# Performance work log

Hardware: AMD Instinct MI355X
Metric: run time of the kernel (lower is better)

## Reference

```python
import jax, jax.numpy as jnp
import numpy as np

B, N, D = 8, 2048, 128
NEG = -9.0e15


def setup_inputs() -> dict:
    key = jax.random.key(0)
    ks = jax.random.split(key, 7)
    x = jax.random.normal(ks[0], (B, N, D), dtype=jnp.float32)
    # sparse-ish binary adjacency with self loops, stored dense as float
    adj = (jax.random.uniform(ks[1], (B, N, N)) < 0.1).astype(jnp.float32)
    adj = jnp.maximum(adj, jnp.eye(N, dtype=jnp.float32)[None])
    s = 1.0 / np.sqrt(D)
    W_w = jax.random.uniform(ks[2], (D, D), minval=-s, maxval=s, dtype=jnp.float32)
    W_b = jax.random.uniform(ks[3], (D,), minval=-s, maxval=s, dtype=jnp.float32)
    A = jnp.zeros((D, D), dtype=jnp.float32) + 0.01 * jax.random.normal(ks[4], (D, D), dtype=jnp.float32)
    s2 = 1.0 / np.sqrt(2 * D)
    gate_w = jax.random.uniform(ks[5], (1, 2 * D), minval=-s2, maxval=s2, dtype=jnp.float32)
    gate_b = jax.random.uniform(ks[6], (1,), minval=-s2, maxval=s2, dtype=jnp.float32)
    return {"x": x, "adj": adj, "W_w": W_w, "W_b": W_b, "A": A,
            "gate_w": gate_w, "gate_b": gate_b}


def reference(x, adj, W_w, W_b, A, gate_w, gate_b):
    # h = W(x): [B,N,D]
    h = jnp.einsum('bnf,df->bnd', x, W_w) + W_b
    # e[b,j,k] = (h A)[b,j,:] . h[b,k,:], then symmetrize
    hA = jnp.einsum('bnd,de->bne', h, A)
    e = jnp.einsum('bjl,bkl->bjk', hA, h)
    e = e + jnp.swapaxes(e, 1, 2)
    att = jnp.where(adj > 0, e, jnp.full_like(e, NEG))
    # NOTE: torch code softmaxes over dim=1 (the j axis)
    att = jax.nn.softmax(att, axis=1)
    att = att * adj
    h_prime = jax.nn.relu(jnp.einsum('bij,bjk->bik', att, h))
    gate_in = jnp.concatenate([x, h_prime], axis=-1)  # [B,N,2D]
    coeff = jax.nn.sigmoid(jnp.einsum('bnc,oc->bno', gate_in, gate_w) + gate_b)  # [B,N,1]
    return coeff * x + (1.0 - coeff) * h_prime
```

## Files before the change

kernel.cpp:

```cpp
#include <hip/hip_runtime.h>


#define B_ 8
#define N_ 2048
#define D_ 128

typedef __attribute__((ext_vector_type(8))) short short8;
typedef __attribute__((ext_vector_type(4))) float f32x4;

#define GLL(gp, lp) __builtin_amdgcn_global_load_lds( \
    (__attribute__((address_space(1))) const unsigned int*)(gp), \
    (__attribute__((address_space(3))) unsigned int*)(lp), 16, 0, 0)

static __device__ __forceinline__ unsigned short f2bf(float f) {
  union { float f; unsigned int u; } v; v.f = f;
  unsigned int r = v.u + 0x7fffu + ((v.u >> 16) & 1u);
  return (unsigned short)(r >> 16);
}
static __device__ __forceinline__ float bf2f(unsigned short u) {
  union { unsigned int u; float f; } v; v.u = ((unsigned int)u) << 16;
  return v.f;
}

#define CAT_OFF ((size_t)0)
#define VT_OFF  ((size_t)8388608)
#define PUN_OFF ((size_t)12582912)
#define S_OFF   ((size_t)79691776)
#define WT_OFF  ((size_t)79757312)

__global__ void k_wt(const float* __restrict__ W, float* __restrict__ Wt) {
  int t = threadIdx.x;
  for (int i = t; i < 128 * 128; i += 256) {
    int d = i >> 7, f = i & 127;
    Wt[f * 128 + d] = W[i];
  }
}

__global__ __launch_bounds__(256) void k1(const float* __restrict__ x,
                                          const float* __restrict__ Wt,
                                          const float* __restrict__ Wb,
                                          const float* __restrict__ A,
                                          unsigned short* __restrict__ cat) {
  __shared__ float xs[8][128];
  __shared__ float hs[8][128];
  const int t = threadIdx.x;
  const size_t rowbase = (size_t)blockIdx.x * 8;
  {
    int row = t >> 5, part = t & 31;
    *(f32x4*)&xs[row][part * 4] = *(const f32x4*)(x + (rowbase + row) * D_ + part * 4);
  }
  __syncthreads();
  const int d = t & 127, r2 = t >> 7;
  float a0 = 0, a1 = 0, a2 = 0, a3 = 0;
  for (int f = 0; f < 128; f++) {
    float wv = Wt[f * 128 + d];
    a0 += xs[r2 * 4 + 0][f] * wv;
    a1 += xs[r2 * 4 + 1][f] * wv;
    a2 += xs[r2 * 4 + 2][f] * wv;
    a3 += xs[r2 * 4 + 3][f] * wv;
  }
  float wb = Wb[d];
  a0 += wb; a1 += wb; a2 += wb; a3 += wb;
  hs[r2 * 4 + 0][d] = a0; hs[r2 * 4 + 1][d] = a1;
  hs[r2 * 4 + 2][d] = a2; hs[r2 * 4 + 3][d] = a3;
  cat[(rowbase + r2 * 4 + 0) * 256 + 128 + d] = f2bf(a0);
  cat[(rowbase + r2 * 4 + 1) * 256 + 128 + d] = f2bf(a1);
  cat[(rowbase + r2 * 4 + 2) * 256 + 128 + d] = f2bf(a2);
  cat[(rowbase + r2 * 4 + 3) * 256 + 128 + d] = f2bf(a3);
  __syncthreads();
  float b0 = 0, b1 = 0, b2 = 0, b3 = 0;
  for (int f = 0; f < 128; f++) {
    float av = A[f * 128 + d];
    b0 += hs[r2 * 4 + 0][f] * av;
    b1 += hs[r2 * 4 + 1][f] * av;
    b2 += hs[r2 * 4 + 2][f] * av;
    b3 += hs[r2 * 4 + 3][f] * av;
  }
  cat[(rowbase + r2 * 4 + 0) * 256 + d] = f2bf(b0);
  cat[(rowbase + r2 * 4 + 1) * 256 + d] = f2bf(b1);
  cat[(rowbase + r2 * 4 + 2) * 256 + d] = f2bf(b2);
  cat[(rowbase + r2 * 4 + 3) * 256 + d] = f2bf(b3);
}

__global__ __launch_bounds__(256, 3) void k2(const unsigned short* __restrict__ cat,
                                             const float* __restrict__ adj,
                                             unsigned short* __restrict__ pun,
                                             float* __restrict__ s_out) {
  __shared__ unsigned short cj[64 * 256];
  const int t = threadIdx.x, w = t >> 6, lane = t & 63;
  const int q = lane >> 4, l15 = lane & 15;
  const int b = blockIdx.z;
  const int kbase = blockIdx.x * 128;
  const int j0b = blockIdx.y * 128;
  const size_t bN = (size_t)b * N_;
  const unsigned short* catp = cat + (bN << 8);
  const int kc = kbase + w * 32;
  short8 brg[2][8];
#pragma unroll
  for (int p = 0; p < 2; p++) {
    int krow = kc + 2 * l15 + p;
#pragma unroll
    for (int m = 0; m < 8; m++)
      brg[p][m] = *(const short8*)(catp + (((size_t)krow) << 8) +
                                   ((((m * 4 + q) + 16) & 31) * 8));
  }
  float acc0 = 0.f, acc1 = 0.f;
  for (int jt = 0; jt < 2; jt++) {
    const int j0 = j0b + jt * 64;
#pragma unroll
    for (int it = 0; it < 8; it++) {
      int sI = it * 256 + t;
      int row = sI >> 5, c = sI & 31;
      GLL(catp + (((size_t)(j0 + row)) << 8) + (c ^ (row & 7)) * 8,
          (char*)cj + sI * 16);
    }
    __syncthreads();
#pragma unroll
    for (int jsub = 0; jsub < 4; jsub++) {
      float2 av[4];
#pragma unroll
      for (int r = 0; r < 4; r++) {
        int jrow = j0 + jsub * 16 + q * 4 + r;
        av[r] = *(const float2*)(adj + (((size_t)(bN + jrow)) << 11) + kc + 2 * l15);
      }
      const int row = jsub * 16 + l15;
      short8 afr[8];
#pragma unroll
      for (int m = 0; m < 8; m++)
        afr[m] = *(short8*)(cj + row * 256 + (((m * 4 + q) ^ (l15 & 7)) * 8));
      f32x4 e0 = {0.f, 0.f, 0.f, 0.f}, e1 = {0.f, 0.f, 0.f, 0.f};
#pragma unroll
      for (int m = 0; m < 8; m++) {
        e0 = __builtin_amdgcn_mfma_f32_16x16x32_bf16(afr[m], brg[0][m], e0, 0, 0, 0);
        e1 = __builtin_amdgcn_mfma_f32_16x16x32_bf16(afr[m], brg[1][m], e1, 0, 0, 0);
      }
#pragma unroll
      for (int r = 0; r < 4; r++) {
        int jrow = j0 + jsub * 16 + q * 4 + r;
        float x0 = av[r].x > 0.f ? __expf(fminf(e0[r], 60.f)) : 0.f;
        float x1 = av[r].y > 0.f ? __expf(fminf(e1[r], 60.f)) : 0.f;
        acc0 += x0; acc1 += x1;
        unsigned int pk = (unsigned int)f2bf(x0) | ((unsigned int)f2bf(x1) << 16);
        *(unsigned int*)(pun + (((size_t)(bN + jrow)) << 11) + kc + 2 * l15) = pk;
      }
    }
    __syncthreads();
  }
  acc0 += __shfl_xor(acc0, 16, 64); acc0 += __shfl_xor(acc0, 32, 64);
  acc1 += __shfl_xor(acc1, 16, 64); acc1 += __shfl_xor(acc1, 32, 64);
  if (lane < 16) {
    atomicAdd(&s_out[bN + kc + 2 * lane], acc0);
    atomicAdd(&s_out[bN + kc + 2 * lane + 1], acc1);
  }
}

__global__ __launch_bounds__(256) void k1v(const unsigned short* __restrict__ cat,
                                           const float* __restrict__ s,
                                           unsigned short* __restrict__ vt) {
  __shared__ unsigned short tile[64][136];
  __shared__ float rsv[64];
  const int t = threadIdx.x;
  const int b = blockIdx.y;
  const int nbase = blockIdx.x * 64;
  if (t < 64) rsv[t] = 1.f / s[(size_t)b * N_ + nbase + t];
#pragma unroll
  for (int k = 0; k < 4; k++) {
    int sI = t + 256 * k;
    int row = sI >> 4, part = sI & 15;
    *(short8*)&tile[row][part * 8] =
        *(const short8*)(cat + (((size_t)(b * N_ + nbase + row)) << 8) + 128 + part * 8);
  }
  __syncthreads();
#pragma unroll
  for (int k = 0; k < 4; k++) {
    int sI = t + 256 * k;
    int dd = sI >> 3, part = sI & 7;
    unsigned short tmp[8];
#pragma unroll
    for (int j = 0; j < 8; j++) {
      int jj = part * 8 + j;
      tmp[j] = f2bf(bf2f(tile[jj][dd]) * rsv[jj]);
    }
    *(short8*)(vt + (((size_t)(b * 128 + dd)) << 11) + nbase + part * 8) = *(short8*)tmp;
  }
}

__global__ __launch_bounds__(256) void k3(const unsigned short* __restrict__ pun,
                                          const unsigned short* __restrict__ vt,
                                          const float* __restrict__ x,
                                          const float* __restrict__ gw,
                                          const float* __restrict__ gb,
                                          float* __restrict__ out) {
  __shared__ char smem[40960];
  const int t = threadIdx.x, w = t >> 6, lane = t & 63;
  const int q = lane >> 4, l15 = lane & 15;
  const int b = blockIdx.y, i0 = blockIdx.x * 32;
  const size_t bN = (size_t)b * N_;
  unsigned short* pa = (unsigned short*)smem;
  unsigned short* vb = (unsigned short*)(smem + 8192);

  f32x4 acc[2][2];
#pragma unroll
  for (int ih = 0; ih < 2; ih++)
#pragma unroll
    for (int dh = 0; dh < 2; dh++) acc[ih][dh] = (f32x4){0.f, 0.f, 0.f, 0.f};

  for (int jt = 0; jt < N_ / 128; jt++) {
    const int j0 = jt * 128;
#pragma unroll
    for (int it = 0; it < 10; it++) {
      int sI = it * 256 + t;
      const unsigned short* g;
      if (sI < 512) {
        int row = sI >> 4, c = sI & 15;
        g = pun + (((size_t)(bN + i0 + row)) << 11) + j0 + ((c ^ (row & 7)) * 8);
      } else {
        int s2 = sI - 512;
        int dd = s2 >> 4, c = s2 & 15;
        g = vt + (((size_t)(b * 128 + dd)) << 11) + j0 + ((c ^ (dd & 7)) * 8);
      }
      GLL(g, smem + sI * 16);
    }
    __syncthreads();
#pragma unroll
    for (int ks = 0; ks < 4; ks++) {
      short8 af[2], bf[2];
#pragma unroll
      for (int ih = 0; ih < 2; ih++) {
        int m = ih * 16 + l15;
        af[ih] = *(short8*)(pa + m * 128 + (((ks * 4 + q) ^ (m & 7)) * 8));
      }
#pragma unroll
      for (int dh = 0; dh < 2; dh++) {
        int d = w * 32 + dh * 16 + l15;
        bf[dh] = *(short8*)(vb + d * 128 + (((ks * 4 + q) ^ (d & 7)) * 8));
      }
      acc[0][0] = __builtin_amdgcn_mfma_f32_16x16x32_bf16(af[0], bf[0], acc[0][0], 0, 0, 0);
      acc[0][1] = __builtin_amdgcn_mfma_f32_16x16x32_bf16(af[0], bf[1], acc[0][1], 0, 0, 0);
      acc[1][0] = __builtin_amdgcn_mfma_f32_16x16x32_bf16(af[1], bf[0], acc[1][0], 0, 0, 0);
      acc[1][1] = __builtin_amdgcn_mfma_f32_16x16x32_bf16(af[1], bf[1], acc[1][1], 0, 0, 0);
    }
    __syncthreads();
  }
  float* hs = (float*)smem;
  float* co = (float*)(smem + 16896);
#pragma unroll
  for (int ih = 0; ih < 2; ih++)
#pragma unroll
    for (int dh = 0; dh < 2; dh++)
#pragma unroll
      for (int r = 0; r < 4; r++) {
        int row = ih * 16 + q * 4 + r;
        int d = w * 32 + dh * 16 + l15;
        hs[row * 132 + d] = fmaxf(acc[ih][dh][r], 0.f);
      }
  __syncthreads();
  {
    int grow = t >> 3, sub = t & 7;
    const float* xr = x + (((size_t)(bN + i0 + grow)) << 7);
    float z = 0.f;
#pragma unroll
    for (int k = 0; k < 16; k++) {
      int dd = sub + 8 * k;
      z += gw[dd] * xr[dd] + gw[128 + dd] * hs[grow * 132 + dd];
    }
    z += __shfl_xor(z, 1, 64);
    z += __shfl_xor(z, 2, 64);
    z += __shfl_xor(z, 4, 64);
    if (sub == 0) co[grow] = 1.f / (1.f + __expf(-(z + gb[0])));
  }
  __syncthreads();
#pragma unroll
  for (int kk = 0; kk < 4; kk++) {
    int id = kk * 256 + t;
    int row = id >> 5, c4 = id & 31;
    size_t g = (((size_t)(bN + i0 + row)) << 7) + c4 * 4;
    f32x4 xv = *(const f32x4*)(x + g);
    f32x4 hv = *(const f32x4*)(hs + row * 132 + c4 * 4);
    float cf = co[row];
    f32x4 o;
#pragma unroll
    for (int e = 0; e < 4; e++) o[e] = cf * xv[e] + (1.f - cf) * hv[e];
    *(f32x4*)(out + g) = o;
  }
}

extern "C" void kernel_launch(void* const* d_in, const int* in_sizes, int n_in,
                              void* d_out, int out_size, void* d_ws, size_t ws_size,
                              hipStream_t stream) {
  const float* x   = (const float*)d_in[0];
  const float* adj = (const float*)d_in[1];
  const float* Ww  = (const float*)d_in[2];
  const float* Wb  = (const float*)d_in[3];
  const float* A   = (const float*)d_in[4];
  const float* gw  = (const float*)d_in[5];
  const float* gb  = (const float*)d_in[6];
  float* out = (float*)d_out;
  char* ws = (char*)d_ws;

  unsigned short* cat = (unsigned short*)(ws + CAT_OFF);
  unsigned short* vt  = (unsigned short*)(ws + VT_OFF);
  unsigned short* pun = (unsigned short*)(ws + PUN_OFF);
  float* s  = (float*)(ws + S_OFF);
  float* Wt = (float*)(ws + WT_OFF);

  hipMemsetAsync(s, 0, (size_t)B_ * N_ * sizeof(float), stream);
  k_wt<<<1, 256, 0, stream>>>(Ww, Wt);
  k1<<<(B_ * N_) / 8, 256, 0, stream>>>(x, Wt, Wb, A, cat);
  k2<<<dim3(N_ / 128, 16, B_), 256, 0, stream>>>(cat, adj, pun, s);
  k1v<<<dim3(N_ / 64, B_), 256, 0, stream>>>(cat, s, vt);
  k3<<<dim3(N_ / 32, B_), 256, 0, stream>>>(pun, vt, x, gw, gb, out);
}
```

Baseline: 310.0 us.

## Drop LDS staging in k2, read j-rows directly and prefetch adjacency

```diff
diff --git a/kernel.cpp b/kernel.cpp
--- a/kernel.cpp
+++ b/kernel.cpp
@@ -82,69 +82,58 @@
   cat[(rowbase + r2 * 4 + 3) * 256 + d] = f2bf(b3);
 }
 
-__global__ __launch_bounds__(256, 3) void k2(const unsigned short* __restrict__ cat,
-                                             const float* __restrict__ adj,
-                                             unsigned short* __restrict__ pun,
-                                             float* __restrict__ s_out) {
-  __shared__ unsigned short cj[64 * 256];
+__global__ __launch_bounds__(256) void k2(const unsigned short* __restrict__ cat,
+                                          const float* __restrict__ adj,
+                                          unsigned short* __restrict__ pun,
+                                          float* __restrict__ s_out) {
   const int t = threadIdx.x, w = t >> 6, lane = t & 63;
   const int q = lane >> 4, l15 = lane & 15;
   const int b = blockIdx.z;
-  const int kbase = blockIdx.x * 128;
-  const int j0b = blockIdx.y * 128;
+  const int kc = (blockIdx.x * 4 + w) * 32;
+  const int j0 = blockIdx.y * 128;
   const size_t bN = (size_t)b * N_;
   const unsigned short* catp = cat + (bN << 8);
-  const int kc = kbase + w * 32;
   short8 brg[2][8];
 #pragma unroll
-  for (int p = 0; p < 2; p++) {
-    int krow = kc + 2 * l15 + p;
+  for (int p = 0; p < 2; p++)
 #pragma unroll
     for (int m = 0; m < 8; m++)
-      brg[p][m] = *(const short8*)(catp + (((size_t)krow) << 8) +
+      brg[p][m] = *(const short8*)(catp + (((size_t)(kc + 2 * l15 + p)) << 8) +
                                    ((((m * 4 + q) + 16) & 31) * 8));
-  }
   float acc0 = 0.f, acc1 = 0.f;
-  for (int jt = 0; jt < 2; jt++) {
-    const int j0 = j0b + jt * 64;
-#pragma unroll
-    for (int it = 0; it < 8; it++) {
-      int sI = it * 256 + t;
-      int row = sI >> 5, c = sI & 31;
-      GLL(catp + (((size_t)(j0 + row)) << 8) + (c ^ (row & 7)) * 8,
-          (char*)cj + sI * 16);
-    }
-    __syncthreads();
-#pragma unroll
-    for (int jsub = 0; jsub < 4; jsub++) {
-      float2 av[4];
-#pragma unroll
-      for (int r = 0; r < 4; r++) {
-        int jrow = j0 + jsub * 16 + q * 4 + r;
-        av[r] = *(const float2*)(adj + (((size_t)(bN + jrow)) << 11) + kc + 2 * l15);
-      }
-      const int row = jsub * 16 + l15;
-      short8 afr[8];
-#pragma unroll
-      for (int m = 0; m < 8; m++)
-        afr[m] = *(short8*)(cj + row * 256 + (((m * 4 + q) ^ (l15 & 7)) * 8));
-      f32x4 e0 = {0.f, 0.f, 0.f, 0.f}, e1 = {0.f, 0.f, 0.f, 0.f};
-#pragma unroll
-      for (int m = 0; m < 8; m++) {
-        e0 = __builtin_amdgcn_mfma_f32_16x16x32_bf16(afr[m], brg[0][m], e0, 0, 0, 0);
-        e1 = __builtin_amdgcn_mfma_f32_16x16x32_bf16(afr[m], brg[1][m], e1, 0, 0, 0);
-      }
-#pragma unroll
-      for (int r = 0; r < 4; r++) {
-        int jrow = j0 + jsub * 16 + q * 4 + r;
-        float x0 = av[r].x > 0.f ? __expf(fminf(e0[r], 60.f)) : 0.f;
-        float x1 = av[r].y > 0.f ? __expf(fminf(e1[r], 60.f)) : 0.f;
-        acc0 += x0; acc1 += x1;
-        unsigned int pk = (unsigned int)f2bf(x0) | ((unsigned int)f2bf(x1) << 16);
-        *(unsigned int*)(pun + (((size_t)(bN + jrow)) << 11) + kc + 2 * l15) = pk;
-      }
-    }
-    __syncthreads();
+  float2 av[4];
+#pragma unroll
+  for (int r = 0; r < 4; r++)
+    av[r] = *(const float2*)(adj + ((bN + j0 + q * 4 + r) << 11) + kc + 2 * l15);
+#pragma unroll 2
+  for (int jsub = 0; jsub < 8; jsub++) {
+    const int jr = j0 + jsub * 16;
+    short8 afr[8];
+#pragma unroll
+    for (int m = 0; m < 8; m++)
+      afr[m] = *(const short8*)(catp + (((size_t)(jr + l15)) << 8) + (m * 4 + q) * 8);
+    f32x4 e0 = {0.f, 0.f, 0.f, 0.f}, e1 = {0.f, 0.f, 0.f, 0.f};
+#pragma unroll
+    for (int m = 0; m < 8; m++) {
+      e0 = __builtin_amdgcn_mfma_f32_16x16x32_bf16(afr[m], brg[0][m], e0, 0, 0, 0);
+      e1 = __builtin_amdgcn_mfma_f32_16x16x32_bf16(afr[m], brg[1][m], e1, 0, 0, 0);
+    }
+    float2 avc[4];
+#pragma unroll
+    for (int r = 0; r < 4; r++) avc[r] = av[r];
+    if (jsub < 7) {
+#pragma unroll
+      for (int r = 0; r < 4; r++)
+        av[r] = *(const float2*)(adj + ((bN + jr + 16 + q * 4 + r) << 11) + kc + 2 * l15);
+    }
+#pragma unroll
+    for (int r = 0; r < 4; r++) {
+      float x0 = avc[r].x > 0.f ? __expf(fminf(e0[r], 60.f)) : 0.f;
+      float x1 = avc[r].y > 0.f ? __expf(fminf(e1[r], 60.f)) : 0.f;
+      acc0 += x0; acc1 += x1;
+      unsigned int pk = (unsigned int)f2bf(x0) | ((unsigned int)f2bf(x1) << 16);
+      *(unsigned int*)(pun + ((bN + jr + q * 4 + r) << 11) + kc + 2 * l15) = pk;
+    }
   }
   acc0 += __shfl_xor(acc0, 16, 64); acc0 += __shfl_xor(acc0, 32, 64);
   acc1 += __shfl_xor(acc1, 16, 64); acc1 += __shfl_xor(acc1, 32, 64);
@@ -307,7 +296,7 @@
   hipMemsetAsync(s, 0, (size_t)B_ * N_ * sizeof(float), stream);
   k_wt<<<1, 256, 0, stream>>>(Ww, Wt);
   k1<<<(B_ * N_) / 8, 256, 0, stream>>>(x, Wt, Wb, A, cat);
-  k2<<<dim3(N_ / 128, 16, B_), 256, 0, stream>>>(cat, adj, pun, s);
+  k2<<<dim3(16, 16, B_), 256, 0, stream>>>(cat, adj, pun, s);
   k1v<<<dim3(N_ / 64, B_), 256, 0, stream>>>(cat, s, vt);
   k3<<<dim3(N_ / 32, B_), 256, 0, stream>>>(pun, vt, x, gw, gb, out);
 }
```

Result: slower. 349.8 us (+12.8%).

## Pack adjacency into bitmask and move projection GEMMs onto bf16 MFMA

Applied to the files above, without the earlier changes.

```diff
diff --git a/kernel.cpp b/kernel.cpp
--- a/kernel.cpp
+++ b/kernel.cpp
@@ -22,68 +22,105 @@
   return v.f;
 }
 
-#define CAT_OFF ((size_t)0)
-#define VT_OFF  ((size_t)8388608)
-#define PUN_OFF ((size_t)12582912)
-#define S_OFF   ((size_t)79691776)
-#define WT_OFF  ((size_t)79757312)
-
-__global__ void k_wt(const float* __restrict__ W, float* __restrict__ Wt) {
+#define CAT_OFF  ((size_t)0)
+#define VT_OFF   ((size_t)8388608)
+#define PUN_OFF  ((size_t)12582912)
+#define S_OFF    ((size_t)79691776)
+#define WB_OFF   ((size_t)79757312)
+#define AT_OFF   ((size_t)79790080)
+#define BITS_OFF ((size_t)79822848)
+
+__global__ void k_cvt(const float* __restrict__ W, const float* __restrict__ A,
+                      unsigned short* __restrict__ Wb1, unsigned short* __restrict__ Abt) {
   int t = threadIdx.x;
   for (int i = t; i < 128 * 128; i += 256) {
-    int d = i >> 7, f = i & 127;
-    Wt[f * 128 + d] = W[i];
-  }
+    Wb1[i] = f2bf(W[i]);
+    Abt[(i & 127) * 128 + (i >> 7)] = f2bf(A[i]);
+  }
+}
+
+__global__ __launch_bounds__(256) void k_bits2(const float* __restrict__ adj,
+                                               unsigned int* __restrict__ bits) {
+  size_t tid = (size_t)blockIdx.x * 256 + threadIdx.x;
+  const float* p = adj + tid * 32;
+  unsigned int m = 0;
+#pragma unroll
+  for (int i = 0; i < 8; i++) {
+    f32x4 v = *(const f32x4*)(p + i * 4);
+    m |= (v[0] > 0.f ? 1u : 0u) << (i * 4 + 0);
+    m |= (v[1] > 0.f ? 1u : 0u) << (i * 4 + 1);
+    m |= (v[2] > 0.f ? 1u : 0u) << (i * 4 + 2);
+    m |= (v[3] > 0.f ? 1u : 0u) << (i * 4 + 3);
+  }
+  bits[tid] = m;
 }
 
 __global__ __launch_bounds__(256) void k1(const float* __restrict__ x,
-                                          const float* __restrict__ Wt,
-                                          const float* __restrict__ Wb,
-                                          const float* __restrict__ A,
+                                          const unsigned short* __restrict__ Wb1,
+                                          const float* __restrict__ Wbias,
+                                          const unsigned short* __restrict__ Abt,
                                           unsigned short* __restrict__ cat) {
-  __shared__ float xs[8][128];
-  __shared__ float hs[8][128];
-  const int t = threadIdx.x;
-  const size_t rowbase = (size_t)blockIdx.x * 8;
-  {
-    int row = t >> 5, part = t & 31;
-    *(f32x4*)&xs[row][part * 4] = *(const f32x4*)(x + (rowbase + row) * D_ + part * 4);
-  }
-  __syncthreads();
-  const int d = t & 127, r2 = t >> 7;
-  float a0 = 0, a1 = 0, a2 = 0, a3 = 0;
-  for (int f = 0; f < 128; f++) {
-    float wv = Wt[f * 128 + d];
-    a0 += xs[r2 * 4 + 0][f] * wv;
-    a1 += xs[r2 * 4 + 1][f] * wv;
-    a2 += xs[r2 * 4 + 2][f] * wv;
-    a3 += xs[r2 * 4 + 3][f] * wv;
-  }
-  float wb = Wb[d];
-  a0 += wb; a1 += wb; a2 += wb; a3 += wb;
-  hs[r2 * 4 + 0][d] = a0; hs[r2 * 4 + 1][d] = a1;
-  hs[r2 * 4 + 2][d] = a2; hs[r2 * 4 + 3][d] = a3;
-  cat[(rowbase + r2 * 4 + 0) * 256 + 128 + d] = f2bf(a0);
-  cat[(rowbase + r2 * 4 + 1) * 256 + 128 + d] = f2bf(a1);
-  cat[(rowbase + r2 * 4 + 2) * 256 + 128 + d] = f2bf(a2);
-  cat[(rowbase + r2 * 4 + 3) * 256 + 128 + d] = f2bf(a3);
-  __syncthreads();
-  float b0 = 0, b1 = 0, b2 = 0, b3 = 0;
-  for (int f = 0; f < 128; f++) {
-    float av = A[f * 128 + d];
-    b0 += hs[r2 * 4 + 0][f] * av;
-    b1 += hs[r2 * 4 + 1][f] * av;
-    b2 += hs[r2 * 4 + 2][f] * av;
-    b3 += hs[r2 * 4 + 3][f] * av;
-  }
-  cat[(rowbase + r2 * 4 + 0) * 256 + d] = f2bf(b0);
-  cat[(rowbase + r2 * 4 + 1) * 256 + d] = f2bf(b1);
-  cat[(rowbase + r2 * 4 + 2) * 256 + d] = f2bf(b2);
-  cat[(rowbase + r2 * 4 + 3) * 256 + d] = f2bf(b3);
+  __shared__ unsigned short hsm[4][16][136];
+  __shared__ unsigned short hasm[4][16][136];
+  const int t = threadIdx.x, w = t >> 6, lane = t & 63;
+  const int q = lane >> 4, l15 = lane & 15;
+  const size_t r0 = (size_t)blockIdx.x * 64 + w * 16;
+
+  f32x4 acc[8];
+#pragma unroll
+  for (int dg = 0; dg < 8; dg++) acc[dg] = (f32x4){0.f, 0.f, 0.f, 0.f};
+#pragma unroll
+  for (int k = 0; k < 4; k++) {
+    const float* xp = x + (r0 + l15) * 128 + k * 32 + q * 8;
+    f32x4 xa = *(const f32x4*)xp;
+    f32x4 xb = *(const f32x4*)(xp + 4);
+    short8 af;
+#pragma unroll
+    for (int e = 0; e < 4; e++) { af[e] = (short)f2bf(xa[e]); af[4 + e] = (short)f2bf(xb[e]); }
+#pragma unroll
+    for (int dg = 0; dg < 8; dg++) {
+      short8 bf = *(const short8*)(Wb1 + (dg * 16 + l15) * 128 + k * 32 + q * 8);
+      acc[dg] = __builtin_amdgcn_mfma_f32_16x16x32_bf16(af, bf, acc[dg], 0, 0, 0);
+    }
+  }
+#pragma unroll
+  for (int dg = 0; dg < 8; dg++) {
+    float bias = Wbias[dg * 16 + l15];
+#pragma unroll
+    for (int r = 0; r < 4; r++)
+      hsm[w][q * 4 + r][dg * 16 + l15] = f2bf(acc[dg][r] + bias);
+  }
+  __syncthreads();
+  f32x4 acc2[8];
+#pragma unroll
+  for (int dg = 0; dg < 8; dg++) acc2[dg] = (f32x4){0.f, 0.f, 0.f, 0.f};
+#pragma unroll
+  for (int k = 0; k < 4; k++) {
+    short8 af = *(short8*)&hsm[w][l15][k * 32 + q * 8];
+#pragma unroll
+    for (int dg = 0; dg < 8; dg++) {
+      short8 bf = *(const short8*)(Abt + (dg * 16 + l15) * 128 + k * 32 + q * 8);
+      acc2[dg] = __builtin_amdgcn_mfma_f32_16x16x32_bf16(af, bf, acc2[dg], 0, 0, 0);
+    }
+  }
+#pragma unroll
+  for (int dg = 0; dg < 8; dg++)
+#pragma unroll
+    for (int r = 0; r < 4; r++)
+      hasm[w][q * 4 + r][dg * 16 + l15] = f2bf(acc2[dg][r]);
+  __syncthreads();
+#pragma unroll
+  for (int it = 0; it < 8; it++) {
+    int idx = it * 64 + lane;
+    int row = idx >> 5, c = idx & 31;
+    short8 v = (c < 16) ? *(short8*)&hasm[w][row][c * 8]
+                        : *(short8*)&hsm[w][row][(c - 16) * 8];
+    *(short8*)(cat + ((r0 + row) << 8) + c * 8) = v;
+  }
 }
 
 __global__ __launch_bounds__(256, 3) void k2(const unsigned short* __restrict__ cat,
-                                             const float* __restrict__ adj,
+                                             const unsigned int* __restrict__ bits,
                                              unsigned short* __restrict__ pun,
                                              float* __restrict__ s_out) {
   __shared__ unsigned short cj[64 * 256];
@@ -95,6 +132,7 @@
   const size_t bN = (size_t)b * N_;
   const unsigned short* catp = cat + (bN << 8);
   const int kc = kbase + w * 32;
+  const int kw = kc >> 5;
   short8 brg[2][8];
 #pragma unroll
   for (int p = 0; p < 2; p++) {
@@ -117,12 +155,6 @@
     __syncthreads();
 #pragma unroll
     for (int jsub = 0; jsub < 4; jsub++) {
-      float2 av[4];
-#pragma unroll
-      for (int r = 0; r < 4; r++) {
-        int jrow = j0 + jsub * 16 + q * 4 + r;
-        av[r] = *(const float2*)(adj + (((size_t)(bN + jrow)) << 11) + kc + 2 * l15);
-      }
       const int row = jsub * 16 + l15;
       short8 afr[8];
 #pragma unroll
@@ -137,11 +169,12 @@
 #pragma unroll
       for (int r = 0; r < 4; r++) {
         int jrow = j0 + jsub * 16 + q * 4 + r;
-        float x0 = av[r].x > 0.f ? __expf(fminf(e0[r], 60.f)) : 0.f;
-        float x1 = av[r].y > 0.f ? __expf(fminf(e1[r], 60.f)) : 0.f;
+        unsigned int mb = bits[(bN + jrow) * 64 + kw];
+        float x0 = ((mb >> (2 * l15)) & 1u) ? __expf(fminf(e0[r], 60.f)) : 0.f;
+        float x1 = ((mb >> (2 * l15 + 1)) & 1u) ? __expf(fminf(e1[r], 60.f)) : 0.f;
         acc0 += x0; acc1 += x1;
         unsigned int pk = (unsigned int)f2bf(x0) | ((unsigned int)f2bf(x1) << 16);
-        *(unsigned int*)(pun + (((size_t)(bN + jrow)) << 11) + kc + 2 * l15) = pk;
+        *(unsigned int*)(pun + ((bN + jrow) << 11) + kc + 2 * l15) = pk;
       }
     }
     __syncthreads();
@@ -302,12 +335,15 @@
   unsigned short* vt  = (unsigned short*)(ws + VT_OFF);
   unsigned short* pun = (unsigned short*)(ws + PUN_OFF);
   float* s  = (float*)(ws + S_OFF);
-  float* Wt = (float*)(ws + WT_OFF);
+  unsigned short* Wb1 = (unsigned short*)(ws + WB_OFF);
+  unsigned short* Abt = (unsigned short*)(ws + AT_OFF);
+  unsigned int* bits  = (unsigned int*)(ws + BITS_OFF);
 
   hipMemsetAsync(s, 0, (size_t)B_ * N_ * sizeof(float), stream);
-  k_wt<<<1, 256, 0, stream>>>(Ww, Wt);
-  k1<<<(B_ * N_) / 8, 256, 0, stream>>>(x, Wt, Wb, A, cat);
-  k2<<<dim3(N_ / 128, 16, B_), 256, 0, stream>>>(cat, adj, pun, s);
+  k_cvt<<<1, 256, 0, stream>>>(Ww, A, Wb1, Abt);
+  k_bits2<<<(B_ * N_ * N_) / (256 * 32), 256, 0, stream>>>(adj, bits);
+  k1<<<(B_ * N_) / 64, 256, 0, stream>>>(x, Wb1, Wb, Abt, cat);
+  k2<<<dim3(N_ / 128, 16, B_), 256, 0, stream>>>(cat, bits, pun, s);
   k1v<<<dim3(N_ / 64, B_), 256, 0, stream>>>(cat, s, vt);
   k3<<<dim3(N_ / 32, B_), 256, 0, stream>>>(pun, vt, x, gw, gb, out);
 }
```

New measurement: 309.0 us. Within noise of the previous version (-0.3%).
